# Kernel optimization log

Measured on AMD Instinct MI355X. Metric: run time of the kernel, lower is better.

## Reference

```python
import jax, jax.numpy as jnp
import numpy as np

N = 100000       # num nodes
E = 1600000      # num edges (avg degree 16)
IN_DIM = 256
EMB_DIM = 128
K = 2            # nlayers: number of propagation steps


def setup_inputs() -> dict:
    key = jax.random.key(0)
    k1, k2, k3, k4, k5 = jax.random.split(key, 5)
    x = jax.random.normal(k1, (N, IN_DIM), dtype=jnp.float32)
    # glorot-initialized linear weight + zero bias
    scale = jnp.sqrt(6.0 / (IN_DIM + EMB_DIM))
    W = jax.random.uniform(k2, (IN_DIM, EMB_DIM), minval=-scale, maxval=scale, dtype=jnp.float32)
    b = jnp.zeros((EMB_DIM,), dtype=jnp.float32)
    edge_src = jax.random.randint(k3, (E,), 0, N, dtype=jnp.int32)
    edge_dst = jax.random.randint(k4, (E,), 0, N, dtype=jnp.int32)
    # normalized-adjacency-like edge weights (positive, ~1/deg scale)
    edge_w = jax.random.uniform(k5, (E,), dtype=jnp.float32) * (1.0 / 16.0)
    return {"x": x, "W": W, "b": b, "edge_src": edge_src, "edge_dst": edge_dst, "edge_w": edge_w}


def reference(x, W, b, edge_src, edge_dst, edge_w):
    # dropout is identity in eval mode; linear + relu
    h = jax.nn.relu(x @ W + b)  # [N, EMB_DIM]
    # k-step sparse propagation: h <- g @ h, g given as COO edge list
    for _ in range(K):
        msg = h[edge_src] * edge_w[:, None]                     # [E, EMB_DIM]
        h = jax.ops.segment_sum(msg, edge_dst, num_segments=N)  # [N, EMB_DIM]
    return h
```

## Files before the change

kernel.cpp:

```cpp
#include <hip/hip_runtime.h>

#define IN_DIM 256
#define EMB 128
#define BKT_SHIFT 9
#define BKT_NODES 512

typedef __attribute__((ext_vector_type(8))) short short8;
typedef __attribute__((ext_vector_type(4))) float f32x4;

__device__ __forceinline__ unsigned short bf16rtne(float f) {
    unsigned int u = __float_as_uint(f);
    return (unsigned short)((u + 0x7fffu + ((u >> 16) & 1u)) >> 16);
}

__device__ __forceinline__ unsigned int packbf2(float lo, float hi) {
    return ((unsigned int)bf16rtne(hi) << 16) | (unsigned int)bf16rtne(lo);
}


__global__ __launch_bounds__(256) void bucket_hist(const int* __restrict__ dst,
                                                   int* __restrict__ ghist, int E) {
    __shared__ int h[256];
    int t = threadIdx.x;
    h[t] = 0;
    __syncthreads();
    int e0 = blockIdx.x * 1024;
    int e1 = min(E, e0 + 1024);
    for (int i = e0 + t; i < e1; i += 256) atomicAdd(&h[dst[i] >> BKT_SHIFT], 1);
    __syncthreads();
    if (h[t]) atomicAdd(&ghist[t], h[t]);
}

__global__ __launch_bounds__(256) void bucket_scan(const int* __restrict__ ghist,
                                                   int* __restrict__ bucket_off,
                                                   int* __restrict__ gcursor,
                                                   int* __restrict__ row_ptr,
                                                   int NB, int N, int E) {
    __shared__ int s[256];
    int t = threadIdx.x;
    int v = (t < NB) ? ghist[t] : 0;
    s[t] = v;
    __syncthreads();
    for (int off = 1; off < 256; off <<= 1) {
        int u = (t >= off) ? s[t - off] : 0;
        __syncthreads();
        s[t] += u;
        __syncthreads();
    }
    int excl = s[t] - v;
    if (t < NB) {
        bucket_off[t] = excl;
        gcursor[t] = excl;
    }
    if (t == 0) {
        bucket_off[NB] = E;
        row_ptr[N] = E;
    }
}


__global__ __launch_bounds__(512) void bin_scatter(const int* __restrict__ src,
                                                   const int* __restrict__ dst,
                                                   const float* __restrict__ w,
                                                   int* __restrict__ gcursor,
                                                   int2* __restrict__ binned, int E) {
    __shared__ int h[256];
    __shared__ int cur[256];
    int t = threadIdx.x;
    if (t < 256) h[t] = 0;
    __syncthreads();
    int e0 = blockIdx.x * 4096;
    int e1 = min(E, e0 + 4096);
    for (int i = e0 + t; i < e1; i += 512) atomicAdd(&h[dst[i] >> BKT_SHIFT], 1);
    __syncthreads();
    if (t < 256) cur[t] = h[t] ? atomicAdd(&gcursor[t], h[t]) : 0;
    __syncthreads();
    for (int i = e0 + t; i < e1; i += 512) {
        int d = dst[i];
        int b = d >> BKT_SHIFT;
        int ld = d & (BKT_NODES - 1);
        int pos = atomicAdd(&cur[b], 1);
        int2 r;
        r.x = src[i] | (ld << 17);
        r.y = __float_as_int(w[i]);
        binned[pos] = r;
    }
}


__global__ __launch_bounds__(1024) void bucket_sort(const int2* __restrict__ binned,
                                                    const int* __restrict__ bucket_off,
                                                    int2* __restrict__ sorted,
                                                    int* __restrict__ row_ptr, int N) {
    __shared__ int cnt[BKT_NODES];
    __shared__ int cur[BKT_NODES];
    __shared__ int scn[BKT_NODES];
    int t = threadIdx.x;
    int b = blockIdx.x;
    int node0 = b << BKT_SHIFT;
    int nn = min(BKT_NODES, N - node0);
    int beg = bucket_off[b];
    int endb = bucket_off[b + 1];
    if (t < BKT_NODES) cnt[t] = 0;
    __syncthreads();
    for (int i = beg + t; i < endb; i += 1024) {
        int ld = ((unsigned int)binned[i].x) >> 17;
        atomicAdd(&cnt[ld], 1);
    }
    __syncthreads();
    int v = 0;
    if (t < BKT_NODES) {
        v = cnt[t];
        scn[t] = v;
    }
    __syncthreads();
    for (int off = 1; off < BKT_NODES; off <<= 1) {
        int u = 0;
        if (t < BKT_NODES && t >= off) u = scn[t - off];
        __syncthreads();
        if (t < BKT_NODES) scn[t] += u;
        __syncthreads();
    }
    if (t < BKT_NODES) {
        int ep = beg + scn[t] - v;
        cur[t] = ep;
        if (t < nn) row_ptr[node0 + t] = ep;
    }
    __syncthreads();
    for (int i = beg + t; i < endb; i += 1024) {
        int2 r = binned[i];
        int ld = ((unsigned int)r.x) >> 17;
        int pos = atomicAdd(&cur[ld], 1);
        r.x &= 0x1FFFF;
        sorted[pos] = r;
    }
}


__global__ __launch_bounds__(256) void wt_cast(const float* __restrict__ W,
                                               unsigned short* __restrict__ wtg) {
    int i = blockIdx.x * 256 + threadIdx.x;
    int c = i & 127;
    int k = i >> 7;
    wtg[c * 256 + k] = bf16rtne(W[(size_t)k * 128 + c]);
}


__global__ __launch_bounds__(256) void gemm_mfma(const float* __restrict__ x,
                                                 const unsigned short* __restrict__ wtg,
                                                 const float* __restrict__ bias,
                                                 unsigned short* __restrict__ hbf, int N) {
    __shared__ unsigned short xs[128][64];
    __shared__ unsigned short wsh[128][64];
    int tid = threadIdx.x;
    int row0 = blockIdx.x * 128;
    int wv = tid >> 6;
    int lane = tid & 63;
    int lr = lane & 15;
    int lg = lane >> 4;
    int wr = wv * 32;

    f32x4 acc[2][8];
#pragma unroll
    for (int m = 0; m < 2; ++m)
#pragma unroll
        for (int n = 0; n < 8; ++n) acc[m][n] = (f32x4){0.f, 0.f, 0.f, 0.f};

    int sr = tid >> 1;
    int hh = tid & 1;
    bool xvalid = (row0 + sr) < N;
    const float* xrow = x + (size_t)(row0 + sr) * IN_DIM + hh * 32;
    const unsigned short* wrow = wtg + (size_t)sr * IN_DIM + hh * 32;

    for (int kb = 0; kb < IN_DIM; kb += 64) {
#pragma unroll
        for (int j = 0; j < 4; ++j) {
            float4 f0 = make_float4(0.f, 0.f, 0.f, 0.f);
            float4 f1 = f0;
            if (xvalid) {
                f0 = ((const float4*)(xrow + kb))[2 * j];
                f1 = ((const float4*)(xrow + kb))[2 * j + 1];
            }
            uint4 pk;
            pk.x = packbf2(f0.x, f0.y);
            pk.y = packbf2(f0.z, f0.w);
            pk.z = packbf2(f1.x, f1.y);
            pk.w = packbf2(f1.z, f1.w);
            int koff = (hh * 32 + j * 8) ^ ((sr & 7) << 3);
            *(uint4*)&xs[sr][koff] = pk;
        }
#pragma unroll
        for (int j = 0; j < 4; ++j) {
            uint4 v = ((const uint4*)(wrow + kb))[j];
            int koff = (hh * 32 + j * 8) ^ ((sr & 7) << 3);
            *(uint4*)&wsh[sr][koff] = v;
        }
        __syncthreads();

        short8 a[2][2];
#pragma unroll
        for (int m = 0; m < 2; ++m)
#pragma unroll
            for (int kk = 0; kk < 2; ++kk) {
                int r = wr + m * 16 + lr;
                int koff = (kk * 32 + lg * 8) ^ ((lr & 7) << 3);
                a[m][kk] = *(const short8*)&xs[r][koff];
            }
#pragma unroll
        for (int n = 0; n < 8; ++n) {
            int c = n * 16 + lr;
            int koff0 = (lg * 8) ^ ((lr & 7) << 3);
            int koff1 = (32 + lg * 8) ^ ((lr & 7) << 3);
            short8 b0 = *(const short8*)&wsh[c][koff0];
            short8 b1 = *(const short8*)&wsh[c][koff1];
            acc[0][n] = __builtin_amdgcn_mfma_f32_16x16x32_bf16(a[0][0], b0, acc[0][n], 0, 0, 0);
            acc[0][n] = __builtin_amdgcn_mfma_f32_16x16x32_bf16(a[0][1], b1, acc[0][n], 0, 0, 0);
            acc[1][n] = __builtin_amdgcn_mfma_f32_16x16x32_bf16(a[1][0], b0, acc[1][n], 0, 0, 0);
            acc[1][n] = __builtin_amdgcn_mfma_f32_16x16x32_bf16(a[1][1], b1, acc[1][n], 0, 0, 0);
        }
        __syncthreads();
    }

#pragma unroll
    for (int n = 0; n < 8; ++n) {
        int c = n * 16 + lr;
        float bv = bias[c];
#pragma unroll
        for (int m = 0; m < 2; ++m) {
#pragma unroll
            for (int j = 0; j < 4; ++j) {
                int r = row0 + wr + m * 16 + lg * 4 + j;
                if (r < N) {
                    float v = fmaxf(acc[m][n][j] + bv, 0.f);
                    hbf[(size_t)r * EMB + c] = bf16rtne(v);
                }
            }
        }
    }
}


template <int OUTBF>
__global__ __launch_bounds__(256) void prop_g(const unsigned int* __restrict__ hin,
                                              void* __restrict__ hout,
                                              const int* __restrict__ rp,
                                              const int2* __restrict__ rec, int N) {
    int wvid = threadIdx.x >> 6;
    int lane = threadIdx.x & 63;
    int node = blockIdx.x * 4 + wvid;
    if (node >= N) return;
    int beg = __builtin_amdgcn_readfirstlane(rp[node]);
    int end = __builtin_amdgcn_readfirstlane(rp[node + 1]);
    float ax = 0.f, ay = 0.f;
    for (int c0 = beg; c0 < end; c0 += 64) {
        int cnt = end - c0;
        if (cnt > 64) cnt = 64;
        int li = lane < cnt ? lane : 0;
        int2 r = rec[c0 + li];
        for (int jb = 0; jb < cnt; jb += 8) {
            int ssrc[8];
            float sw[8];
#pragma unroll
            for (int k = 0; k < 8; ++k) {
                int jj = jb + k;
                int jc = jj < cnt ? jj : 0;
                ssrc[k] = __builtin_amdgcn_readlane(r.x, jc);
                float wv = __uint_as_float((unsigned int)__builtin_amdgcn_readlane(r.y, jc));
                sw[k] = (jj < cnt) ? wv : 0.f;
            }
            unsigned int g[8];
#pragma unroll
            for (int k = 0; k < 8; ++k) g[k] = hin[(size_t)ssrc[k] * 64 + lane];
#pragma unroll
            for (int k = 0; k < 8; ++k) {
                ax = fmaf(sw[k], __uint_as_float(g[k] << 16), ax);
                ay = fmaf(sw[k], __uint_as_float(g[k] & 0xffff0000u), ay);
            }
        }
    }
    if (OUTBF) {
        ((unsigned int*)hout)[(size_t)node * 64 + lane] = packbf2(ax, ay);
    } else {
        float2 o;
        o.x = ax;
        o.y = ay;
        ((float2*)hout)[(size_t)node * 64 + lane] = o;
    }
}


extern "C" void kernel_launch(void* const* d_in, const int* in_sizes, int n_in,
                              void* d_out, int out_size, void* d_ws, size_t ws_size,
                              hipStream_t stream) {
    const float* x = (const float*)d_in[0];
    const float* W = (const float*)d_in[1];
    const float* b = (const float*)d_in[2];
    const int* esrc = (const int*)d_in[3];
    const int* edst = (const int*)d_in[4];
    const float* ew = (const float*)d_in[5];
    int N = in_sizes[0] / IN_DIM;
    int E = in_sizes[3];
    int NB = (N + BKT_NODES - 1) >> BKT_SHIFT;

    char* p = (char*)d_ws;
    auto alloc = [&](size_t bytes) -> void* {
        void* r = (void*)p;
        p += (bytes + 255) & ~(size_t)255;
        return r;
    };
    unsigned short* hbf = (unsigned short*)alloc((size_t)N * EMB * 2);
    unsigned short* h1bf = (unsigned short*)alloc((size_t)N * EMB * 2);
    unsigned short* wtg = (unsigned short*)alloc((size_t)IN_DIM * EMB * 2);
    int* ghist = (int*)alloc(256 * 4);
    int* gcursor = (int*)alloc(256 * 4);
    int* bucket_off = (int*)alloc((size_t)(NB + 1) * 4);
    int* row_ptr = (int*)alloc((size_t)(N + 1) * 4);
    int2* binned = (int2*)alloc((size_t)E * 8);
    int2* sorted = (int2*)alloc((size_t)E * 8);

    hipMemsetAsync(ghist, 0, 256 * 4, stream);
    bucket_hist<<<(E + 1023) / 1024, 256, 0, stream>>>(edst, ghist, E);
    bucket_scan<<<1, 256, 0, stream>>>(ghist, bucket_off, gcursor, row_ptr, NB, N, E);
    bin_scatter<<<(E + 4095) / 4096, 512, 0, stream>>>(esrc, edst, ew, gcursor, binned, E);
    bucket_sort<<<NB, 1024, 0, stream>>>(binned, bucket_off, sorted, row_ptr, N);

    wt_cast<<<(IN_DIM * EMB) / 256, 256, 0, stream>>>(W, wtg);
    gemm_mfma<<<(N + 127) / 128, 256, 0, stream>>>(x, wtg, b, hbf, N);
    prop_g<1><<<(N + 3) / 4, 256, 0, stream>>>((const unsigned int*)hbf, h1bf, row_ptr, sorted, N);
    prop_g<0><<<(N + 3) / 4, 256, 0, stream>>>((const unsigned int*)h1bf, d_out, row_ptr, sorted, N);
}
```

Baseline: 250.8 us.

## Stream x directly into MFMA registers and preload full W tile in LDS

The GEMM now loads the full bf16 weight matrix into shared memory once per block and drops the x staging tile. Each lane loads its own x fragments straight from global memory into registers, converts them with hardware packed bf16 conversion, and prefetches the next K-slice while the current one runs on MFMA. This removes the per-step syncthreads and the LDS round-trip for x. The cost is 64KB of LDS per block, which may limit occupancy, and x loads that are less coalesced. wt_cast is also moved earlier in the stream, which does not change the work done.

```diff
diff --git a/kernel.cpp b/kernel.cpp
--- a/kernel.cpp
+++ b/kernel.cpp
@@ -15,6 +15,15 @@
 
 __device__ __forceinline__ unsigned int packbf2(float lo, float hi) {
     return ((unsigned int)bf16rtne(hi) << 16) | (unsigned int)bf16rtne(lo);
+}
+
+__device__ __forceinline__ short8 pack8(float4 f0, float4 f1) {
+    union { uint4 u; short8 s; } U;
+    asm("v_cvt_pk_bf16_f32 %0, %1, %2" : "=v"(U.u.x) : "v"(f0.x), "v"(f0.y));
+    asm("v_cvt_pk_bf16_f32 %0, %1, %2" : "=v"(U.u.y) : "v"(f0.z), "v"(f0.w));
+    asm("v_cvt_pk_bf16_f32 %0, %1, %2" : "=v"(U.u.z) : "v"(f1.x), "v"(f1.y));
+    asm("v_cvt_pk_bf16_f32 %0, %1, %2" : "=v"(U.u.w) : "v"(f1.z), "v"(f1.w));
+    return U.s;
 }
 
 
@@ -150,8 +159,7 @@
                                                  const unsigned short* __restrict__ wtg,
                                                  const float* __restrict__ bias,
                                                  unsigned short* __restrict__ hbf, int N) {
-    __shared__ unsigned short xs[128][64];
-    __shared__ unsigned short wsh[128][64];
+    __shared__ unsigned short wsh[128][256];
     int tid = threadIdx.x;
     int row0 = blockIdx.x * 128;
     int wv = tid >> 6;
@@ -160,66 +168,77 @@
     int lg = lane >> 4;
     int wr = wv * 32;
 
+    int r0 = row0 + wr + lr;
+    int r1 = r0 + 16;
+    bool v0 = r0 < N, v1 = r1 < N;
+    const float* xr0 = x + (size_t)r0 * IN_DIM;
+    const float* xr1 = x + (size_t)r1 * IN_DIM;
+    const float4 zf4 = make_float4(0.f, 0.f, 0.f, 0.f);
+
+    float4 bufA[4][2], bufB[4][2];
+#pragma unroll
+    for (int m = 0; m < 2; ++m)
+#pragma unroll
+        for (int kk = 0; kk < 2; ++kk) {
+            const float* src = (m ? xr1 : xr0) + kk * 32 + lg * 8;
+            bool ok = m ? v1 : v0;
+            bufA[m * 2 + kk][0] = ok ? ((const float4*)src)[0] : zf4;
+            bufA[m * 2 + kk][1] = ok ? ((const float4*)src)[1] : zf4;
+        }
+
+#pragma unroll
+    for (int it = 0; it < 16; ++it) {
+        int cidx = it * 256 + tid;
+        int c = cidx >> 5;
+        int k0 = (cidx & 31) * 8;
+        int koff = k0 ^ ((c & 7) << 3);
+        uint4 v = *(const uint4*)(wtg + c * 256 + k0);
+        *(uint4*)&wsh[c][koff] = v;
+    }
+
     f32x4 acc[2][8];
 #pragma unroll
     for (int m = 0; m < 2; ++m)
 #pragma unroll
         for (int n = 0; n < 8; ++n) acc[m][n] = (f32x4){0.f, 0.f, 0.f, 0.f};
 
-    int sr = tid >> 1;
-    int hh = tid & 1;
-    bool xvalid = (row0 + sr) < N;
-    const float* xrow = x + (size_t)(row0 + sr) * IN_DIM + hh * 32;
-    const unsigned short* wrow = wtg + (size_t)sr * IN_DIM + hh * 32;
-
-    for (int kb = 0; kb < IN_DIM; kb += 64) {
-#pragma unroll
-        for (int j = 0; j < 4; ++j) {
-            float4 f0 = make_float4(0.f, 0.f, 0.f, 0.f);
-            float4 f1 = f0;
-            if (xvalid) {
-                f0 = ((const float4*)(xrow + kb))[2 * j];
-                f1 = ((const float4*)(xrow + kb))[2 * j + 1];
-            }
-            uint4 pk;
-            pk.x = packbf2(f0.x, f0.y);
-            pk.y = packbf2(f0.z, f0.w);
-            pk.z = packbf2(f1.x, f1.y);
-            pk.w = packbf2(f1.z, f1.w);
-            int koff = (hh * 32 + j * 8) ^ ((sr & 7) << 3);
-            *(uint4*)&xs[sr][koff] = pk;
-        }
-#pragma unroll
-        for (int j = 0; j < 4; ++j) {
-            uint4 v = ((const uint4*)(wrow + kb))[j];
-            int koff = (hh * 32 + j * 8) ^ ((sr & 7) << 3);
-            *(uint4*)&wsh[sr][koff] = v;
-        }
-        __syncthreads();
-
+    __syncthreads();
+
+    auto body = [&](int kt, float4 (&cur)[4][2], float4 (&nxt)[4][2], bool pf) {
+        if (pf) {
+#pragma unroll
+            for (int m = 0; m < 2; ++m)
+#pragma unroll
+                for (int kk = 0; kk < 2; ++kk) {
+                    const float* src = (m ? xr1 : xr0) + (kt + 1) * 64 + kk * 32 + lg * 8;
+                    bool ok = m ? v1 : v0;
+                    nxt[m * 2 + kk][0] = ok ? ((const float4*)src)[0] : zf4;
+                    nxt[m * 2 + kk][1] = ok ? ((const float4*)src)[1] : zf4;
+                }
+        }
         short8 a[2][2];
 #pragma unroll
         for (int m = 0; m < 2; ++m)
 #pragma unroll
-            for (int kk = 0; kk < 2; ++kk) {
-                int r = wr + m * 16 + lr;
-                int koff = (kk * 32 + lg * 8) ^ ((lr & 7) << 3);
-                a[m][kk] = *(const short8*)&xs[r][koff];
-            }
+            for (int kk = 0; kk < 2; ++kk)
+                a[m][kk] = pack8(cur[m * 2 + kk][0], cur[m * 2 + kk][1]);
 #pragma unroll
         for (int n = 0; n < 8; ++n) {
             int c = n * 16 + lr;
-            int koff0 = (lg * 8) ^ ((lr & 7) << 3);
-            int koff1 = (32 + lg * 8) ^ ((lr & 7) << 3);
-            short8 b0 = *(const short8*)&wsh[c][koff0];
-            short8 b1 = *(const short8*)&wsh[c][koff1];
+            int sw = (c & 7) << 3;
+            short8 b0 = *(const short8*)&wsh[c][(kt * 64 + lg * 8) ^ sw];
+            short8 b1 = *(const short8*)&wsh[c][(kt * 64 + 32 + lg * 8) ^ sw];
             acc[0][n] = __builtin_amdgcn_mfma_f32_16x16x32_bf16(a[0][0], b0, acc[0][n], 0, 0, 0);
             acc[0][n] = __builtin_amdgcn_mfma_f32_16x16x32_bf16(a[0][1], b1, acc[0][n], 0, 0, 0);
             acc[1][n] = __builtin_amdgcn_mfma_f32_16x16x32_bf16(a[1][0], b0, acc[1][n], 0, 0, 0);
             acc[1][n] = __builtin_amdgcn_mfma_f32_16x16x32_bf16(a[1][1], b1, acc[1][n], 0, 0, 0);
         }
-        __syncthreads();
-    }
+    };
+
+    body(0, bufA, bufB, true);
+    body(1, bufB, bufA, true);
+    body(2, bufA, bufB, true);
+    body(3, bufB, bufA, false);
 
 #pragma unroll
     for (int n = 0; n < 8; ++n) {
@@ -319,12 +338,12 @@
     int2* sorted = (int2*)alloc((size_t)E * 8);
 
     hipMemsetAsync(ghist, 0, 256 * 4, stream);
+    wt_cast<<<(IN_DIM * EMB) / 256, 256, 0, stream>>>(W, wtg);
     bucket_hist<<<(E + 1023) / 1024, 256, 0, stream>>>(edst, ghist, E);
     bucket_scan<<<1, 256, 0, stream>>>(ghist, bucket_off, gcursor, row_ptr, NB, N, E);
     bin_scatter<<<(E + 4095) / 4096, 512, 0, stream>>>(esrc, edst, ew, gcursor, binned, E);
     bucket_sort<<<NB, 1024, 0, stream>>>(binned, bucket_off, sorted, row_ptr, N);
 
-    wt_cast<<<(IN_DIM * EMB) / 256, 256, 0, stream>>>(W, wtg);
     gemm_mfma<<<(N + 127) / 128, 256, 0, stream>>>(x, wtg, b, hbf, N);
     prop_g<1><<<(N + 3) / 4, 256, 0, stream>>>((const unsigned int*)hbf, h1bf, row_ptr, sorted, N);
     prop_g<0><<<(N + 3) / 4, 256, 0, stream>>>((const unsigned int*)h1bf, d_out, row_ptr, sorted, N);
```

Result: slower. 278.9 us (+11.2%).
